# Kernel optimization log

Measured on AMD Instinct MI355X. Metric: run time of the kernel, lower is better.

Reference implementation:

```python
import jax, jax.numpy as jnp
import numpy as np

N_STATIC, N_DYNAMIC = 64, 32
INPUT_DIM = N_STATIC + N_DYNAMIC * 9 + 8   # 360
EMBED = 64
HIDDEN = 2048
OUT = 512
T = 4096
L_IN0 = INPUT_DIM + EMBED                   # 424


def setup_inputs() -> dict:
    key = jax.random.key(0)
    ks = jax.random.split(key, 11)
    s = lambda k, shape: jax.random.normal(k, shape, jnp.float32) * 0.02
    return {
        "inputVecs": jax.random.normal(ks[0], (T, INPUT_DIM), jnp.float32),
        "Wih0": s(ks[1], (4 * HIDDEN, L_IN0)),
        "bih0": s(ks[2], (4 * HIDDEN,)),
        "bhh0": s(ks[3], (4 * HIDDEN,)),
        "Wih1": s(ks[4], (4 * HIDDEN, HIDDEN)),
        "bih1": s(ks[5], (4 * HIDDEN,)),
        "bhh1": s(ks[6], (4 * HIDDEN,)),
        "Wlin": s(ks[7], (OUT, HIDDEN)),
        "blin": s(ks[8], (OUT,)),
        "Wmap": s(ks[9], (EMBED, OUT)),
        "bmap": s(ks[10], (EMBED,)),
        "embed0": jnp.zeros((EMBED,), jnp.float32),
    }


def _cell(gates):
    # PyTorch LSTM gate order: input, forget, cell(g), output.
    # h0 = c0 = 0 each step -> c = sigmoid(i)*tanh(g), h = sigmoid(o)*tanh(c).
    i, f, g, o = jnp.split(gates, 4)
    c = jax.nn.sigmoid(i) * jnp.tanh(g)
    return jax.nn.sigmoid(o) * jnp.tanh(c)


def reference(inputVecs, Wih0, bih0, bhh0, Wih1, bih1, bhh1, Wlin, blin, Wmap, bmap, embed0):
    # The original calls nn.LSTM without hx every timestep, so PyTorch uses
    # zero initial (h, c): all W_hh @ h terms vanish; only b_hh biases remain.
    # The sole cross-time recurrence is the embed feedback loop.
    D = inputVecs.shape[1]
    Wx, We = Wih0[:, :D], Wih0[:, D:]
    # Hoist the large input GEMM out of the scan: (T, 4H)
    gates_x = inputVecs @ Wx.T + (bih0 + bhh0)
    b1 = bih1 + bhh1

    def step(embed, gx):
        h0 = _cell(gx + We @ embed)              # LSTM layer 0 (single step)
        h1 = _cell(Wih1 @ h0 + b1)               # LSTM layer 1 (single step)
        y = Wlin @ h1 + blin                     # (OUT,)  == linear(lstm_out)
        new_embed = Wmap @ jax.nn.log_softmax(y) + bmap  # map(log_softmax(y))
        return new_embed, y

    _, ys = jax.lax.scan(step, embed0, gates_x)
    return ys                                     # (T, OUT) stacked outputs
```

## Files before the change

### kernel.cpp

```cpp
#include <hip/hip_runtime.h>

#define GWG 256
#define BTH 768
#define WROW 2052
#define LDSZ 137856
#define TB   0x5AB00001

typedef float f4v __attribute__((ext_vector_type(4)));

__device__ __forceinline__ unsigned short b16(float f) {
  union { float f; unsigned int i; } z; z.f = f;
  unsigned int r = z.i + 0x7fffu + ((z.i >> 16) & 1u);
  return (unsigned short)(r >> 16);
}
__device__ __forceinline__ float bup(unsigned short u) {
  union { unsigned int i; float f; } z; z.i = ((unsigned int)u) << 16; return z.f;
}
__device__ __forceinline__ float blo(unsigned int p) {
  union { unsigned int i; float f; } z; z.i = p << 16; return z.f;
}
__device__ __forceinline__ float bhi(unsigned int p) {
  union { unsigned int i; float f; } z; z.i = p & 0xffff0000u; return z.f;
}
__device__ __forceinline__ float sigm(float x) { return 1.f / (1.f + expf(-x)); }

__device__ __forceinline__ void stG(float* p2, f4v v) {
  asm volatile("global_store_dwordx4 %0, %1, off sc0 sc1" :: "v"(p2), "v"(v) : "memory");
}

__device__ __forceinline__ void pollH(const float* mb, int tag, unsigned short* lHb) {
  const int L = threadIdx.x;
  const float* base = mb + L * 4;
  f4v v[8];
  for (;;) {
#pragma unroll
    for (int s = 0; s < 8; ++s)
      asm volatile("global_load_dwordx4 %0, %1, off sc0 sc1"
                   : "=v"(v[s]) : "v"(base + s * 256) : "memory");
    asm volatile("s_waitcnt vmcnt(0)" ::: "memory");
    __builtin_amdgcn_sched_barrier(0);
    bool ok = true;
#pragma unroll
    for (int s = 0; s < 8; ++s) ok &= (__float_as_int(v[s][3]) == tag);
    if (__all(ok)) break;
    __builtin_amdgcn_s_sleep(1);
  }
#pragma unroll
  for (int s = 0; s < 8; ++s) {
    int c = s * 64 + L;
    uint2 u; u.x = __float_as_uint(v[s][0]); u.y = __float_as_uint(v[s][1]);
    *(uint2*)&lHb[c * 4] = u;
  }
}

__global__ __launch_bounds__(256) void prep(const float* __restrict__ bih0, const float* __restrict__ bhh0,
                                            const float* __restrict__ bih1, const float* __restrict__ bhh1,
                                            float* __restrict__ b0, float* __restrict__ b1f) {
  int i = blockIdx.x * 256 + threadIdx.x;
  if (i < 8192) { b0[i] = bih0[i] + bhh0[i]; b1f[i] = bih1[i] + bhh1[i]; }
}

__global__ __launch_bounds__(256) void transpose_wx(const float* __restrict__ Wih0, float* __restrict__ WxT) {
  int idx = blockIdx.x * 256 + threadIdx.x;
  int r = idx & 8191, k = idx >> 13;
  WxT[(size_t)k * 8192 + r] = Wih0[(size_t)r * 424 + k];
}

__global__ __launch_bounds__(256) void gemm_gx(const float* __restrict__ inV, const float* __restrict__ WxT,
                                               const float* __restrict__ b0, unsigned short* __restrict__ gxb) {
  __shared__ float lin[32 * 360];
  int t0 = blockIdx.x * 32;
  int by = blockIdx.y;
  int ry = by >> 3;
  int gatey = ry + (ry ? 1 : 0);
  int r  = gatey * 2048 + (by & 7) * 256 + threadIdx.x;
  int cr = ry    * 2048 + (by & 7) * 256 + threadIdx.x;
  for (int i = threadIdx.x; i < 32 * 360; i += 256) lin[i] = inV[(size_t)t0 * 360 + i];
  __syncthreads();
  float b = b0[r];
  float acc[32];
#pragma unroll
  for (int tt = 0; tt < 32; ++tt) acc[tt] = b;
  for (int k = 0; k < 360; k += 4) {
    float w0 = WxT[(size_t)(k + 0) * 8192 + r];
    float w1 = WxT[(size_t)(k + 1) * 8192 + r];
    float w2 = WxT[(size_t)(k + 2) * 8192 + r];
    float w3 = WxT[(size_t)(k + 3) * 8192 + r];
#pragma unroll
    for (int tt = 0; tt < 32; ++tt) {
      float4 l = *reinterpret_cast<const float4*>(&lin[tt * 360 + k]);
      acc[tt] = fmaf(w0, l.x, fmaf(w1, l.y, fmaf(w2, l.z, fmaf(w3, l.w, acc[tt]))));
    }
  }
  for (int tt = 0; tt < 32; ++tt) gxb[(size_t)(t0 + tt) * 6144 + cr] = b16(acc[tt]);
}

__global__ __launch_bounds__(256) void wcomb_k(const float* __restrict__ Wih0, const float* __restrict__ Wmap,
                                               unsigned short* __restrict__ wcomb) {
  __shared__ float lwe[64];
  int cr = blockIdx.x;
  int orig = cr + (cr >= 2048 ? 2048 : 0);
  if (threadIdx.x < 64) lwe[threadIdx.x] = Wih0[(size_t)orig * 424 + 360 + threadIdx.x];
  __syncthreads();
  int c = threadIdx.x;
  float a0 = 0.f, a1 = 0.f;
  for (int e = 0; e < 64; ++e) {
    float w = lwe[e];
    a0 = fmaf(w, Wmap[e * 512 + c], a0);
    a1 = fmaf(w, Wmap[e * 512 + c + 256], a1);
  }
  wcomb[(size_t)cr * 512 + c] = b16(a0);
  wcomb[(size_t)cr * 512 + c + 256] = b16(a1);
}

__global__ __launch_bounds__(256) void rsk(const unsigned short* __restrict__ wcomb,
                                           const float* __restrict__ Wih0,
                                           const float* __restrict__ bmap, const float* __restrict__ emb0,
                                           float* __restrict__ rs, float* __restrict__ bcomb,
                                           float* __restrict__ g0c) {
  int cr = blockIdx.x * 256 + threadIdx.x;
  if (cr >= 6144) return;
  int orig = cr + (cr >= 2048 ? 2048 : 0);
  float s = 0.f;
  for (int k = 0; k < 512; ++k) s += bup(wcomb[(size_t)cr * 512 + k]);
  float bc = 0.f, g0 = 0.f;
  for (int e = 0; e < 64; ++e) {
    float w = Wih0[(size_t)orig * 424 + 360 + e];
    bc = fmaf(w, bmap[e], bc);
    g0 = fmaf(w, emb0[e], g0);
  }
  rs[cr] = s; bcomb[cr] = bc; g0c[cr] = g0;
}

struct KP {
  const float* Wih1; const float* Wlin; const float* blin; const float* b1f;
  const unsigned short* gxb; const unsigned short* wcomb;
  const float* rs; const float* bcomb; const float* g0c;
  float* mb_h0; float* mb_h1; float* mb_y;
  float* out;
};

__global__ __launch_bounds__(BTH) void lstm_seq(KP p) {
  extern __shared__ __align__(16) char smem[];
  unsigned short* lW1  = (unsigned short*)smem;
  unsigned short* lWl  = (unsigned short*)(smem + 98496);
  unsigned short* lWcb = (unsigned short*)(smem + 106688);
  unsigned short* lHb  = (unsigned short*)(smem + 131264);
  float* lY  = (float*)(smem + 135360);
  float* lRA = (float*)(smem + 137408);
  float* lRS = (float*)(smem + 137536);
  float* lR  = (float*)(smem + 137664);
  float* lV  = (float*)(smem + 137792);

  const int w = blockIdx.x, tid = threadIdx.x;
  const int rl = tid >> 5;
  const int l32 = tid & 31;
  const int g3 = rl >> 3;
  const int gate = g3 + (g3 ? 1 : 0);
  const int gr  = w * 8 + (rl & 7) + 2048 * gate;
  const int crt = w * 8 + (rl & 7) + 2048 * g3;
  const int rep = w & 7;

  for (int r2 = 0; r2 < 24; ++r2) {
    int gg = r2 >> 3; int grr = w * 8 + (r2 & 7) + 2048 * (gg + (gg ? 1 : 0));
    const float* src = p.Wih1 + (size_t)grr * 2048;
    for (int i = tid; i < 2048; i += BTH) lW1[r2 * WROW + i] = b16(src[i]);
  }
  for (int i = tid; i < 24 * 512; i += BTH) {
    int r2 = i >> 9, k = i & 511;
    int crr = w * 8 + (r2 & 7) + 2048 * (r2 >> 3);
    lWcb[r2 * 512 + k] = p.wcomb[(size_t)crr * 512 + k];
  }
  for (int i = tid; i < 2 * 2048; i += BTH) {
    int q = i >> 11, k = i & 2047;
    lWl[i] = b16(p.Wlin[(size_t)(w * 2 + q) * 2048 + k]);
  }
  const float b1r  = p.b1f[gr];
  const float rs_r = p.rs[crt], bc_r = p.bcomb[crt], g0_r = p.g0c[crt];
  const float bl0 = p.blin[w * 2], bl1 = p.blin[w * 2 + 1];
  unsigned short gxu = p.gxb[crt];
  if (l32 == 0) lRS[rl] = rs_r;
  __syncthreads();

  for (int t = 0; t < 4096; ++t) {
    const int tagt = TB + t;
    const unsigned short gxu_n = p.gxb[(size_t)(t < 4095 ? t + 1 : t) * 6144 + crt];
    float lse = 0.f;
    if (t > 0) {
      f4v yv[4];
      if (tid < 64) {
        const float* base = p.mb_y + rep * 1024 + tid * 4;
        for (;;) {
#pragma unroll
          for (int s = 0; s < 4; ++s)
            asm volatile("global_load_dwordx4 %0, %1, off sc0 sc1"
                         : "=v"(yv[s]) : "v"(base + s * 256) : "memory");
          asm volatile("s_waitcnt vmcnt(0)" ::: "memory");
          __builtin_amdgcn_sched_barrier(0);
          bool ok = true;
#pragma unroll
          for (int s = 0; s < 4; ++s) ok &= (__float_as_int(yv[s][3]) == tagt - 1);
          if (__all(ok)) break;
          __builtin_amdgcn_s_sleep(1);
        }
#pragma unroll
        for (int s = 0; s < 4; ++s) {
          int c = s * 64 + tid;
          lY[c * 2] = yv[s][0]; lY[c * 2 + 1] = yv[s][1];
        }
      }
      __syncthreads();
      if (tid < 64) {
        float s = 0.f;
#pragma unroll
        for (int q = 0; q < 4; ++q) s += expf(yv[q][0]) + expf(yv[q][1]);
#pragma unroll
        for (int d = 1; d < 64; d <<= 1) s += __shfl_xor(s, d);
        lse = logf(s);
      }
      float acc = 0.f;
#pragma unroll
      for (int j = 0; j < 8; ++j) {
        int k = 2 * l32 + 64 * j;
        unsigned uwp = *(const unsigned*)&lWcb[rl * 512 + k];
        float2 yv2 = *(const float2*)&lY[k];
        acc = fmaf(blo(uwp), yv2.x, fmaf(bhi(uwp), yv2.y, acc));
      }
      acc += __shfl_xor(acc, 1); acc += __shfl_xor(acc, 2); acc += __shfl_xor(acc, 4);
      acc += __shfl_xor(acc, 8); acc += __shfl_xor(acc, 16);
      if (l32 == 0) lRA[rl] = bup(gxu) + acc + bc_r;
    } else {
      if (l32 == 0) lRA[rl] = bup(gxu) + g0_r;
    }
    __syncthreads();
    if (tid < 16) {
      unsigned hb = 0u;
      if (tid < 8) {
        float pi = lRA[tid]      - lse * lRS[tid];
        float pg = lRA[8 + tid]  - lse * lRS[8 + tid];
        float po = lRA[16 + tid] - lse * lRS[16 + tid];
        float cc = sigm(pi) * tanhf(pg);
        hb = (unsigned)b16(sigm(po) * tanhf(cc));
      }
      int cpar = tid & 1;
      unsigned a0 = __shfl(hb, cpar * 4 + 0);
      unsigned a1 = __shfl(hb, cpar * 4 + 1);
      unsigned a2 = __shfl(hb, cpar * 4 + 2);
      unsigned a3 = __shfl(hb, cpar * 4 + 3);
      f4v c;
      c[0] = __uint_as_float(a0 | (a1 << 16));
      c[1] = __uint_as_float(a2 | (a3 << 16));
      c[2] = 0.f; c[3] = __int_as_float(tagt);
      stG(p.mb_h0 + (tid >> 1) * 2048 + (w * 2 + cpar) * 4, c);
    }
    if (tid < 64) pollH(p.mb_h0 + rep * 2048, tagt, lHb);
    __syncthreads();
    {
      float acc = 0.f;
      const unsigned short* wr = lW1 + rl * WROW;
#pragma unroll 4
      for (int mm = 0; mm < 16; ++mm) {
        int k = l32 * 4 + mm * 128;
        ushort4 uw = *(const ushort4*)&wr[k];
        ushort4 uh = *(const ushort4*)&lHb[k];
        acc = fmaf(bup(uw.x), bup(uh.x), acc);
        acc = fmaf(bup(uw.y), bup(uh.y), acc);
        acc = fmaf(bup(uw.z), bup(uh.z), acc);
        acc = fmaf(bup(uw.w), bup(uh.w), acc);
      }
      acc += __shfl_xor(acc, 1); acc += __shfl_xor(acc, 2); acc += __shfl_xor(acc, 4);
      acc += __shfl_xor(acc, 8); acc += __shfl_xor(acc, 16);
      if (l32 == 0) lR[rl] = acc + b1r;
    }
    __syncthreads();
    if (tid < 16) {
      unsigned hb = 0u;
      if (tid < 8) {
        float cc = sigm(lR[tid]) * tanhf(lR[8 + tid]);
        hb = (unsigned)b16(sigm(lR[16 + tid]) * tanhf(cc));
      }
      int cpar = tid & 1;
      unsigned a0 = __shfl(hb, cpar * 4 + 0);
      unsigned a1 = __shfl(hb, cpar * 4 + 1);
      unsigned a2 = __shfl(hb, cpar * 4 + 2);
      unsigned a3 = __shfl(hb, cpar * 4 + 3);
      f4v c;
      c[0] = __uint_as_float(a0 | (a1 << 16));
      c[1] = __uint_as_float(a2 | (a3 << 16));
      c[2] = 0.f; c[3] = __int_as_float(tagt);
      stG(p.mb_h1 + (tid >> 1) * 2048 + (w * 2 + cpar) * 4, c);
    }
    if (tid < 64) pollH(p.mb_h1 + rep * 2048, tagt, lHb);
    __syncthreads();
    if (tid < 512) {
      int q = tid >> 8, l = tid & 255;
      float a = 0.f;
#pragma unroll
      for (int it = 0; it < 2; ++it) {
        int k = it * 1024 + l * 4;
        ushort4 uw = *(const ushort4*)&lWl[q * 2048 + k];
        ushort4 uh = *(const ushort4*)&lHb[k];
        a = fmaf(bup(uw.x), bup(uh.x), a);
        a = fmaf(bup(uw.y), bup(uh.y), a);
        a = fmaf(bup(uw.z), bup(uh.z), a);
        a = fmaf(bup(uw.w), bup(uh.w), a);
      }
#pragma unroll
      for (int d = 1; d < 64; d <<= 1) a += __shfl_xor(a, d);
      if ((tid & 63) == 0) lV[tid >> 6] = a;
    }
    __syncthreads();
    if (tid < 8) {
      float y0 = lV[0] + lV[1] + lV[2] + lV[3] + bl0;
      float y1 = lV[4] + lV[5] + lV[6] + lV[7] + bl1;
      f4v c; c[0] = y0; c[1] = y1; c[2] = 0.f; c[3] = __int_as_float(tagt);
      stG(p.mb_y + tid * 1024 + w * 4, c);
      if (tid == 0) {
        p.out[(size_t)t * 512 + w * 2]     = y0;
        p.out[(size_t)t * 512 + w * 2 + 1] = y1;
      }
    }
    gxu = gxu_n;
  }
}

extern "C" void kernel_launch(void* const* d_in, const int* in_sizes, int n_in,
                              void* d_out, int out_size, void* d_ws, size_t ws_size,
                              hipStream_t stream) {
  const float* inV  = (const float*)d_in[0];
  const float* Wih0 = (const float*)d_in[1];
  const float* bih0 = (const float*)d_in[2];
  const float* bhh0 = (const float*)d_in[3];
  const float* Wih1 = (const float*)d_in[4];
  const float* bih1 = (const float*)d_in[5];
  const float* bhh1 = (const float*)d_in[6];
  const float* Wlin = (const float*)d_in[7];
  const float* blin = (const float*)d_in[8];
  const float* Wmap = (const float*)d_in[9];
  const float* bmap = (const float*)d_in[10];
  const float* emb0 = (const float*)d_in[11];

  char* ws = (char*)d_ws;
  unsigned short* gxb   = (unsigned short*)(ws);
  float*          WxT   = (float*)(ws + 50331648);
  unsigned short* wcomb = (unsigned short*)(ws + 50331648);
  float* b0    = (float*)(ws + 62128128);
  float* b1f   = (float*)(ws + 62160896);
  float* mb_h0 = (float*)(ws + 62193664);
  float* mb_h1 = (float*)(ws + 62259200);
  float* mb_y  = (float*)(ws + 62324736);
  float* rs    = (float*)(ws + 62357504);
  float* bcomb = (float*)(ws + 62382080);
  float* g0c   = (float*)(ws + 62406656);
  float* out   = (float*)d_out;

  prep<<<32, 256, 0, stream>>>(bih0, bhh0, bih1, bhh1, b0, b1f);
  transpose_wx<<<11520, 256, 0, stream>>>(Wih0, WxT);
  gemm_gx<<<dim3(128, 24), 256, 0, stream>>>(inV, WxT, b0, gxb);
  wcomb_k<<<6144, 256, 0, stream>>>(Wih0, Wmap, wcomb);
  rsk<<<24, 256, 0, stream>>>(wcomb, Wih0, bmap, emb0, rs, bcomb, g0c);

  hipFuncSetAttribute(reinterpret_cast<const void*>(lstm_seq),
                      hipFuncAttributeMaxDynamicSharedMemorySize, LDSZ);
  KP p{Wih1, Wlin, blin, b1f, gxb, wcomb, rs, bcomb, g0c, mb_h0, mb_h1, mb_y, out};
  void* args[] = { (void*)&p };
  hipError_t e = hipLaunchCooperativeKernel(reinterpret_cast<void*>(&lstm_seq),
                                            dim3(GWG), dim3(BTH), args, LDSZ, stream);
  if (e != hipSuccess) {
    lstm_seq<<<GWG, BTH, LDSZ, stream>>>(p);
  }
}
```

Measured before the change: 31.25 ms.

## Fuse output reduction, precompute exp per y, store hidden state as fp32 in LDS

Each block now computes its two output values with one wave each and a full wave reduction, which removes the extra __syncthreads and the partial-sum LDS stage in the linear layer. The producer also publishes exp(y) next to y in the mailbox, so consumers only sum precomputed exponentials for the log-sum-exp instead of running expf on every received value. Received hidden states are unpacked from bf16 to fp32 once into LDS, so the inner dot products avoid repeated conversion. In exchange LDS use grows, the y mailbox grows to one float4 per output, and each consumer polling wave reads twice as many mailbox lines.

New measurement: 31.06 ms. About the same (-0.6%).

```diff
diff --git a/kernel.cpp b/kernel.cpp
--- a/kernel.cpp
+++ b/kernel.cpp
@@ -3,7 +3,7 @@
 #define GWG 256
 #define BTH 768
 #define WROW 2052
-#define LDSZ 137856
+#define LDSZ 141888
 #define TB   0x5AB00001
 
 typedef float f4v __attribute__((ext_vector_type(4)));
@@ -28,7 +28,7 @@
   asm volatile("global_store_dwordx4 %0, %1, off sc0 sc1" :: "v"(p2), "v"(v) : "memory");
 }
 
-__device__ __forceinline__ void pollH(const float* mb, int tag, unsigned short* lHb) {
+__device__ __forceinline__ void pollH(const float* mb, int tag, float* lH) {
   const int L = threadIdx.x;
   const float* base = mb + L * 4;
   f4v v[8];
@@ -48,9 +48,40 @@
 #pragma unroll
   for (int s = 0; s < 8; ++s) {
     int c = s * 64 + L;
-    uint2 u; u.x = __float_as_uint(v[s][0]); u.y = __float_as_uint(v[s][1]);
-    *(uint2*)&lHb[c * 4] = u;
-  }
+    unsigned u0 = __float_as_uint(v[s][0]);
+    unsigned u1 = __float_as_uint(v[s][1]);
+    f4v hw; hw[0] = blo(u0); hw[1] = bhi(u0); hw[2] = blo(u1); hw[3] = bhi(u1);
+    *(f4v*)&lH[c * 4] = hw;
+  }
+}
+
+__device__ __forceinline__ float pollYE(const float* mb, int tag, float* lY) {
+  const int L = threadIdx.x;
+  const float* base = mb + L * 4;
+  f4v v[8];
+  for (;;) {
+#pragma unroll
+    for (int s = 0; s < 8; ++s)
+      asm volatile("global_load_dwordx4 %0, %1, off sc0 sc1"
+                   : "=v"(v[s]) : "v"(base + s * 256) : "memory");
+    asm volatile("s_waitcnt vmcnt(0)" ::: "memory");
+    __builtin_amdgcn_sched_barrier(0);
+    bool ok = true;
+#pragma unroll
+    for (int s = 0; s < 8; ++s) ok &= (__float_as_int(v[s][3]) == tag);
+    if (__all(ok)) break;
+    __builtin_amdgcn_s_sleep(1);
+  }
+  float es = 0.f;
+#pragma unroll
+  for (int s = 0; s < 8; ++s) {
+    int c = s * 64 + L;
+    lY[c] = v[s][0];
+    es += v[s][1];
+  }
+#pragma unroll
+  for (int d = 1; d < 64; d <<= 1) es += __shfl_xor(es, d);
+  return logf(es);
 }
 
 __global__ __launch_bounds__(256) void prep(const float* __restrict__ bih0, const float* __restrict__ bhh0,
@@ -145,12 +176,11 @@
   unsigned short* lW1  = (unsigned short*)smem;
   unsigned short* lWl  = (unsigned short*)(smem + 98496);
   unsigned short* lWcb = (unsigned short*)(smem + 106688);
-  unsigned short* lHb  = (unsigned short*)(smem + 131264);
-  float* lY  = (float*)(smem + 135360);
-  float* lRA = (float*)(smem + 137408);
-  float* lRS = (float*)(smem + 137536);
-  float* lR  = (float*)(smem + 137664);
-  float* lV  = (float*)(smem + 137792);
+  float* lH  = (float*)(smem + 131264);
+  float* lY  = (float*)(smem + 139456);
+  float* lRA = (float*)(smem + 141504);
+  float* lRS = (float*)(smem + 141632);
+  float* lR  = (float*)(smem + 141760);
 
   const int w = blockIdx.x, tid = threadIdx.x;
   const int rl = tid >> 5;
@@ -160,6 +190,8 @@
   const int gr  = w * 8 + (rl & 7) + 2048 * gate;
   const int crt = w * 8 + (rl & 7) + 2048 * g3;
   const int rep = w & 7;
+  const int wv  = tid >> 6;
+  const int L64 = tid & 63;
 
   for (int r2 = 0; r2 < 24; ++r2) {
     int gg = r2 >> 3; int grr = w * 8 + (r2 & 7) + 2048 * (gg + (gg ? 1 : 0));
@@ -177,7 +209,7 @@
   }
   const float b1r  = p.b1f[gr];
   const float rs_r = p.rs[crt], bc_r = p.bcomb[crt], g0_r = p.g0c[crt];
-  const float bl0 = p.blin[w * 2], bl1 = p.blin[w * 2 + 1];
+  const float blr  = (wv < 2) ? p.blin[w * 2 + wv] : 0.f;
   unsigned short gxu = p.gxb[crt];
   if (l32 == 0) lRS[rl] = rs_r;
   __syncthreads();
@@ -187,37 +219,8 @@
     const unsigned short gxu_n = p.gxb[(size_t)(t < 4095 ? t + 1 : t) * 6144 + crt];
     float lse = 0.f;
     if (t > 0) {
-      f4v yv[4];
-      if (tid < 64) {
-        const float* base = p.mb_y + rep * 1024 + tid * 4;
-        for (;;) {
-#pragma unroll
-          for (int s = 0; s < 4; ++s)
-            asm volatile("global_load_dwordx4 %0, %1, off sc0 sc1"
-                         : "=v"(yv[s]) : "v"(base + s * 256) : "memory");
-          asm volatile("s_waitcnt vmcnt(0)" ::: "memory");
-          __builtin_amdgcn_sched_barrier(0);
-          bool ok = true;
-#pragma unroll
-          for (int s = 0; s < 4; ++s) ok &= (__float_as_int(yv[s][3]) == tagt - 1);
-          if (__all(ok)) break;
-          __builtin_amdgcn_s_sleep(1);
-        }
-#pragma unroll
-        for (int s = 0; s < 4; ++s) {
-          int c = s * 64 + tid;
-          lY[c * 2] = yv[s][0]; lY[c * 2 + 1] = yv[s][1];
-        }
-      }
+      if (tid < 64) lse = pollYE(p.mb_y + rep * 2048, tagt - 1, lY);
       __syncthreads();
-      if (tid < 64) {
-        float s = 0.f;
-#pragma unroll
-        for (int q = 0; q < 4; ++q) s += expf(yv[q][0]) + expf(yv[q][1]);
-#pragma unroll
-        for (int d = 1; d < 64; d <<= 1) s += __shfl_xor(s, d);
-        lse = logf(s);
-      }
       float acc = 0.f;
 #pragma unroll
       for (int j = 0; j < 8; ++j) {
@@ -253,7 +256,7 @@
       c[2] = 0.f; c[3] = __int_as_float(tagt);
       stG(p.mb_h0 + (tid >> 1) * 2048 + (w * 2 + cpar) * 4, c);
     }
-    if (tid < 64) pollH(p.mb_h0 + rep * 2048, tagt, lHb);
+    if (tid < 64) pollH(p.mb_h0 + rep * 2048, tagt, lH);
     __syncthreads();
     {
       float acc = 0.f;
@@ -262,11 +265,11 @@
       for (int mm = 0; mm < 16; ++mm) {
         int k = l32 * 4 + mm * 128;
         ushort4 uw = *(const ushort4*)&wr[k];
-        ushort4 uh = *(const ushort4*)&lHb[k];
-        acc = fmaf(bup(uw.x), bup(uh.x), acc);
-        acc = fmaf(bup(uw.y), bup(uh.y), acc);
-        acc = fmaf(bup(uw.z), bup(uh.z), acc);
-        acc = fmaf(bup(uw.w), bup(uh.w), acc);
+        float4 hv = *(const float4*)&lH[k];
+        acc = fmaf(bup(uw.x), hv.x, acc);
+        acc = fmaf(bup(uw.y), hv.y, acc);
+        acc = fmaf(bup(uw.z), hv.z, acc);
+        acc = fmaf(bup(uw.w), hv.w, acc);
       }
       acc += __shfl_xor(acc, 1); acc += __shfl_xor(acc, 2); acc += __shfl_xor(acc, 4);
       acc += __shfl_xor(acc, 8); acc += __shfl_xor(acc, 16);
@@ -290,35 +293,27 @@
       c[2] = 0.f; c[3] = __int_as_float(tagt);
       stG(p.mb_h1 + (tid >> 1) * 2048 + (w * 2 + cpar) * 4, c);
     }
-    if (tid < 64) pollH(p.mb_h1 + rep * 2048, tagt, lHb);
+    if (tid < 64) pollH(p.mb_h1 + rep * 2048, tagt, lH);
     __syncthreads();
-    if (tid < 512) {
-      int q = tid >> 8, l = tid & 255;
+    if (wv < 2) {
       float a = 0.f;
 #pragma unroll
-      for (int it = 0; it < 2; ++it) {
-        int k = it * 1024 + l * 4;
-        ushort4 uw = *(const ushort4*)&lWl[q * 2048 + k];
-        ushort4 uh = *(const ushort4*)&lHb[k];
-        a = fmaf(bup(uw.x), bup(uh.x), a);
-        a = fmaf(bup(uw.y), bup(uh.y), a);
-        a = fmaf(bup(uw.z), bup(uh.z), a);
-        a = fmaf(bup(uw.w), bup(uh.w), a);
+      for (int i = 0; i < 8; ++i) {
+        int k = L64 * 4 + i * 256;
+        ushort4 uw = *(const ushort4*)&lWl[wv * 2048 + k];
+        float4 hv = *(const float4*)&lH[k];
+        a = fmaf(bup(uw.x), hv.x, fmaf(bup(uw.y), hv.y,
+              fmaf(bup(uw.z), hv.z, fmaf(bup(uw.w), hv.w, a))));
       }
 #pragma unroll
       for (int d = 1; d < 64; d <<= 1) a += __shfl_xor(a, d);
-      if ((tid & 63) == 0) lV[tid >> 6] = a;
-    }
-    __syncthreads();
-    if (tid < 8) {
-      float y0 = lV[0] + lV[1] + lV[2] + lV[3] + bl0;
-      float y1 = lV[4] + lV[5] + lV[6] + lV[7] + bl1;
-      f4v c; c[0] = y0; c[1] = y1; c[2] = 0.f; c[3] = __int_as_float(tagt);
-      stG(p.mb_y + tid * 1024 + w * 4, c);
-      if (tid == 0) {
-        p.out[(size_t)t * 512 + w * 2]     = y0;
-        p.out[(size_t)t * 512 + w * 2 + 1] = y1;
-      }
+      float y = a + blr;
+      float e = expf(y);
+      if (L64 < 8) {
+        f4v c; c[0] = y; c[1] = e; c[2] = 0.f; c[3] = __int_as_float(tagt);
+        stG(p.mb_y + L64 * 2048 + (w * 2 + wv) * 4, c);
+      }
+      if (L64 == 0) p.out[(size_t)t * 512 + w * 2 + wv] = y;
     }
     gxu = gxu_n;
   }
@@ -349,9 +344,9 @@
   float* mb_h0 = (float*)(ws + 62193664);
   float* mb_h1 = (float*)(ws + 62259200);
   float* mb_y  = (float*)(ws + 62324736);
-  float* rs    = (float*)(ws + 62357504);
-  float* bcomb = (float*)(ws + 62382080);
-  float* g0c   = (float*)(ws + 62406656);
+  float* rs    = (float*)(ws + 62390272);
+  float* bcomb = (float*)(ws + 62414848);
+  float* g0c   = (float*)(ws + 62439424);
   float* out   = (float*)d_out;
 
   prep<<<32, 256, 0, stream>>>(bih0, bhh0, bih1, bhh1, b0, b1f);
```
